# Performance work log

Hardware: AMD Instinct MI355X
Metric: run time of the kernel (lower is better)

## Reference

```python
import jax, jax.numpy as jnp
import numpy as np


def setup_inputs() -> dict:
    key = jax.random.key(0)
    kq, kk, kv = jax.random.split(key, 3)
    B, H, T, D = 2, 8, 8192, 64
    return {
        "Q": jax.random.normal(kq, (B, H, T, D), dtype=jnp.float32),
        "K": jax.random.normal(kk, (B, H, T, D), dtype=jnp.float32),
        "V": jax.random.normal(kv, (B, H, T, D), dtype=jnp.float32),
        "window_size": 512,
    }


def _gather_bands(x, nb, Wn):
    # x: [B,H,T,D] -> [B,H,nb,3*Wn,D], key blocks (i-1, i, i+1) per query block i
    B, H, T, D = x.shape
    xb = x.reshape(B, H, nb, Wn, D)
    xp = jnp.pad(xb, ((0, 0), (0, 0), (1, 1), (0, 0), (0, 0)))
    return jnp.concatenate([xp[:, :, i:i + nb] for i in range(3)], axis=3)


def reference(Q, K, V, window_size):
    # Sliding-window attention: softmax over keys with |q_idx - kv_idx| <= window_size,
    # computed block-sparsely (only the 3 neighboring key blocks per query block).
    B, H, T, D = Q.shape
    Wn = int(window_size)
    assert T % Wn == 0
    nb = T // Wn
    scale = 1.0 / (D ** 0.5)

    Qb = Q.reshape(B, H, nb, Wn, D)
    Kw = _gather_bands(K, nb, Wn)  # [B,H,nb,3W,D]
    Vw = _gather_bands(V, nb, Wn)

    # scores within the band: [B,H,nb,W,3W]
    s = jnp.einsum('bhnqd,bhnkd->bhnqk', Qb, Kw) * scale

    # exact band mask: global q = n*W + q_loc, global kv = (n-1)*W + k_loc
    q_loc = jnp.arange(Wn)[:, None]
    k_loc = jnp.arange(3 * Wn)[None, :]
    band = jnp.abs(q_loc + Wn - k_loc) <= Wn          # [W, 3W]
    kv_g = (jnp.arange(nb)[:, None] - 1) * Wn + jnp.arange(3 * Wn)[None, :]  # [nb, 3W]
    valid = (kv_g >= 0) & (kv_g < T)
    mask = band[None, :, :] & valid[:, None, :]        # [nb, W, 3W]

    s = jnp.where(mask[None, None], s, -jnp.inf)
    p = jax.nn.softmax(s, axis=-1)
    o = jnp.einsum('bhnqk,bhnkd->bhnqd', p, Vw)
    return o.reshape(B, H, T, D)
```

## Files before the change

### kernel.cpp

```cpp
#include <hip/hip_runtime.h>
#include <hip/hip_bf16.h>
#include <stdint.h>

typedef __attribute__((ext_vector_type(8))) short bf16x8;
typedef __attribute__((ext_vector_type(4))) short bf16x4;
typedef __attribute__((ext_vector_type(4))) float f32x4;

#define T_SEQ   8192
#define D_HEAD  64
#define NHEADS  16
#define WIN     512
#define BQ      128
#define BK      64
#define NTILES  (T_SEQ / BK)
#define TILE_E  (BK * D_HEAD)
#define LDSR    72
#define MASKVAL (-1.0e6f)

#define WS_NEEDED ((size_t)2 * NHEADS * T_SEQ * D_HEAD * 2)

#define MFMA16(a,b,c) __builtin_amdgcn_mfma_f32_16x16x16bf16_1k(a,b,c,0,0,0)

extern "C" __device__ __attribute__((const)) float __ocml_native_exp2_f32(float);
__device__ __forceinline__ float fexp2(float x) { return __ocml_native_exp2_f32(x); }

#define GLDS16(g, l) __builtin_amdgcn_global_load_lds( \
    (const __attribute__((address_space(1))) void*)(g), \
    (__attribute__((address_space(3))) void*)(l), 16, 0, 0)

__device__ __forceinline__ short f2bf(float f) {
    union { float f; uint32_t u; } v; v.f = f;
    return (short)((v.u + 0x7FFFu + ((v.u >> 16) & 1u)) >> 16);
}

__device__ __forceinline__ uint32_t pkbf2(float lo, float hi) {
    union { __hip_bfloat162 h; uint32_t u; } c;
    c.h = __float22bfloat162_rn(make_float2(lo, hi));
    return c.u;
}

__global__ __launch_bounds__(256, 2)
void prep_kv(const float* __restrict__ Kg, const float* __restrict__ Vg,
             short* __restrict__ Kb, short* __restrict__ Vt)
{
    __shared__ float vt[64 * 65];
    const int tid  = threadIdx.x;
    const int tile = blockIdx.x & (NTILES - 1);
    const int head = blockIdx.x >> 7;
    const size_t off = ((size_t)head * T_SEQ + (size_t)tile * BK) * D_HEAD;

    const float* ks = Kg + off;
    short* kd = Kb + off;
    #pragma unroll
    for (int i = 0; i < 2; ++i) {
        int L = tid + 256 * i;
        int row = L >> 3, c = L & 7;
        const float* s = ks + row * 64 + c * 8;
        float4 a = *(const float4*)s;
        float4 b = *(const float4*)(s + 4);
        short out[8] = { f2bf(a.x), f2bf(a.y), f2bf(a.z), f2bf(a.w),
                         f2bf(b.x), f2bf(b.y), f2bf(b.z), f2bf(b.w) };
        *(bf16x8*)(kd + (row * 8 + (c ^ (row & 7))) * 8) = *(bf16x8*)out;
    }

    const float* vs = Vg + off;
    #pragma unroll
    for (int i = 0; i < 4; ++i) {
        int idx = tid + 256 * i;
        int row = idx >> 4, c4 = (idx & 15) << 2;
        float4 v = *(const float4*)(vs + row * D_HEAD + c4);
        *(float4*)&vt[row * 65 + c4] = v;
    }
    __syncthreads();
    short* vd = Vt + ((size_t)head * NTILES + tile) * TILE_E;
    {
        int d = tid >> 2, q = tid & 3;
        #pragma unroll
        for (int h = 0; h < 2; ++h) {
            int c = h * 4 + q;
            short out[8];
            #pragma unroll
            for (int j = 0; j < 4; ++j) out[j]     = f2bf(vt[(h*32      + q*4 + j) * 65 + d]);
            #pragma unroll
            for (int j = 0; j < 4; ++j) out[4 + j] = f2bf(vt[(h*32 + 16 + q*4 + j) * 65 + d]);
            *(bf16x8*)(vd + (d * 8 + (c ^ (d & 7))) * 8) = *(bf16x8*)out;
        }
    }
}

__global__ __launch_bounds__(256, 4)
void swa_fwd(const float* __restrict__ Qg, const short* __restrict__ Kb,
             const short* __restrict__ Vt, float* __restrict__ Og)
{
    __shared__ short Ks[2][TILE_E];
    __shared__ short Vs[2][TILE_E];

    const int tid  = threadIdx.x;
    const int wave = tid >> 6;
    const int lane = tid & 63;
    const int lcol = lane & 15;
    const int quad = lane >> 4;
    const int rx   = lcol & 7;

    const int g    = blockIdx.x;
    const int head = g >> 6;
    const int qt   = ((g & 7) << 3) | ((g >> 3) & 7);
    const int q0   = qt * BQ;
    const int tq   = q0 >> 6;

    const float* Qp = Qg + (size_t)head * T_SEQ * D_HEAD;
    const short* Kp = Kb + (size_t)head * T_SEQ * D_HEAD;
    float*       Op = Og + (size_t)head * T_SEQ * D_HEAD;

    const float qscale = 0.125f * 1.44269504088896340736f;
    const int qrow_w = q0 + wave * 32;

    bf16x8 qf[2][2];
    #pragma unroll
    for (int mt = 0; mt < 2; ++mt) {
        const float* qptr = Qp + (size_t)(qrow_w + mt*16 + lcol) * D_HEAD + quad * 8;
        #pragma unroll
        for (int ks = 0; ks < 2; ++ks) {
            float4 a = *(const float4*)(qptr + ks*32);
            float4 b = *(const float4*)(qptr + ks*32 + 4);
            bf16x8 f;
            f[0]=f2bf(a.x*qscale); f[1]=f2bf(a.y*qscale); f[2]=f2bf(a.z*qscale); f[3]=f2bf(a.w*qscale);
            f[4]=f2bf(b.x*qscale); f[5]=f2bf(b.y*qscale); f[6]=f2bf(b.z*qscale); f[7]=f2bf(b.w*qscale);
            qf[mt][ks] = f;
        }
    }

    f32x4 oacc[2][4];
    f32x4 lacc[2];
    const f32x4 zero4 = {0.f, 0.f, 0.f, 0.f};
    const short oneb = (short)0x3F80;
    const bf16x4 ones4 = {oneb, oneb, oneb, oneb};
    #pragma unroll
    for (int mt = 0; mt < 2; ++mt) {
        lacc[mt] = zero4;
        #pragma unroll
        for (int nt = 0; nt < 4; ++nt) oacc[mt][nt] = zero4;
    }

    int t0 = (q0 - WIN) >> 6;            if (t0 < 0) t0 = 0;
    int t1 = (q0 + BQ - 1 + WIN) >> 6;   if (t1 > NTILES - 1) t1 = NTILES - 1;

    const int ch0 = wave * 2, ch1 = wave * 2 + 1;

    {
        const short* ksrc = Kp + (size_t)t0 * TILE_E;
        const short* vsrc = Vt + ((size_t)head * NTILES + t0) * TILE_E;
        GLDS16(ksrc + ch0*512 + lane*8, &Ks[0][ch0*512]);
        GLDS16(ksrc + ch1*512 + lane*8, &Ks[0][ch1*512]);
        GLDS16(vsrc + ch0*512 + lane*8, &Vs[0][ch0*512]);
        GLDS16(vsrc + ch1*512 + lane*8, &Vs[0][ch1*512]);
    }
    asm volatile("s_waitcnt vmcnt(0)" ::: "memory");
    __syncthreads();

    int p = 0;
    for (int t = t0; t <= t1; ++t) {
        {
            const int tn = (t + 1 <= t1) ? t + 1 : t1;
            const short* ksrc = Kp + (size_t)tn * TILE_E;
            const short* vsrc = Vt + ((size_t)head * NTILES + tn) * TILE_E;
            short* kds = &Ks[p^1][0];
            short* vds = &Vs[p^1][0];
            GLDS16(ksrc + ch0*512 + lane*8, kds + ch0*512);
            GLDS16(ksrc + ch1*512 + lane*8, kds + ch1*512);
            GLDS16(vsrc + ch0*512 + lane*8, vds + ch0*512);
            GLDS16(vsrc + ch1*512 + lane*8, vds + ch1*512);
        }

        const short* Kcur = &Ks[p][0];
        const short* Vcur = &Vs[p][0];
        const bool edge = (t < tq - 6) || (t > tq + 7);

        #pragma unroll
        for (int h = 0; h < 2; ++h) {
            bf16x8 vv[4];
            #pragma unroll
            for (int nt = 0; nt < 4; ++nt)
                vv[nt] = *(const bf16x8*)&Vcur[(nt*16 + lcol)*64 + (((h*4 + quad) ^ rx) << 3)];

            f32x4 sc[2][2];
            #pragma unroll
            for (int j = 0; j < 2; ++j) { sc[j][0] = zero4; sc[j][1] = zero4; }
            #pragma unroll
            for (int ks = 0; ks < 2; ++ks) {
                #pragma unroll
                for (int j = 0; j < 2; ++j) {
                    bf16x8 kf = *(const bf16x8*)&Kcur[((2*h+j)*16 + lcol)*64
                                                      + (((ks*4 + quad) ^ rx) << 3)];
                    sc[j][0] = __builtin_amdgcn_mfma_f32_16x16x32_bf16(kf, qf[0][ks], sc[j][0], 0,0,0);
                    sc[j][1] = __builtin_amdgcn_mfma_f32_16x16x32_bf16(kf, qf[1][ks], sc[j][1], 0,0,0);
                }
            }

            if (edge) {
                #pragma unroll
                for (int j = 0; j < 2; ++j) {
                    const int kg0 = t*BK + (2*h+j)*16 + quad*4;
                    #pragma unroll
                    for (int mt = 0; mt < 2; ++mt) {
                        const int qg = qrow_w + mt*16 + lcol;
                        #pragma unroll
                        for (int r = 0; r < 4; ++r) {
                            int dq = qg - (kg0 + r);
                            if (dq > WIN || dq < -WIN) sc[j][mt][r] = MASKVAL;
                        }
                    }
                }
            }

            #pragma unroll
            for (int j = 0; j < 2; ++j) {
                bf16x4 vh[4];
                #pragma unroll
                for (int nt = 0; nt < 4; ++nt) {
                    bf16x8 v8 = vv[nt];
                    bf16x4 x = { v8[j*4+0], v8[j*4+1], v8[j*4+2], v8[j*4+3] };
                    vh[nt] = x;
                }
                #pragma unroll
                for (int mt = 0; mt < 2; ++mt) {
                    float p0 = fexp2(sc[j][mt][0]);
                    float p1 = fexp2(sc[j][mt][1]);
                    float p2 = fexp2(sc[j][mt][2]);
                    float p3 = fexp2(sc[j][mt][3]);
                    union { int2 i; bf16x4 v; } pf;
                    pf.i = make_int2((int)pkbf2(p0, p1), (int)pkbf2(p2, p3));
                    lacc[mt] = MFMA16(ones4, pf.v, lacc[mt]);
                    #pragma unroll
                    for (int nt = 0; nt < 4; ++nt)
                        oacc[mt][nt] = MFMA16(vh[nt], pf.v, oacc[mt][nt]);
                }
            }
        }

        asm volatile("s_waitcnt vmcnt(0)" ::: "memory");
        __syncthreads();
        p ^= 1;
    }

    #pragma unroll
    for (int mt = 0; mt < 2; ++mt) {
        float inv = 1.0f / lacc[mt][0];
        const int qg = qrow_w + mt*16 + lcol;
        float* op = Op + (size_t)qg * D_HEAD + quad*4;
        #pragma unroll
        for (int nt = 0; nt < 4; ++nt) {
            float4 o = { oacc[mt][nt][0]*inv, oacc[mt][nt][1]*inv,
                         oacc[mt][nt][2]*inv, oacc[mt][nt][3]*inv };
            *(float4*)(op + nt*16) = o;
        }
    }
}

#define BQF     128
__global__ __launch_bounds__(256, 4)
void swa_fused_fb(const float* __restrict__ Qg, const float* __restrict__ Kg,
                  const float* __restrict__ Vg, float* __restrict__ Og)
{
    __shared__ short Ksf[BK * LDSR];
    __shared__ short Vsf[D_HEAD * LDSR];
    __shared__ float Vtmp[BK * 65];

    const int tid  = threadIdx.x;
    const int wave = tid >> 6;
    const int lane = tid & 63;
    const int lcol = lane & 15;
    const int quad = lane >> 4;

    const int g    = blockIdx.x;
    const int head = g >> 6;
    const int qt   = ((g & 7) << 3) | ((g >> 3) & 7);
    const int q0   = qt * BQF;
    const int tq   = q0 >> 6;

    const size_t hoff = (size_t)head * T_SEQ * D_HEAD;
    const float* Qp = Qg + hoff;
    const float* Kp = Kg + hoff;
    const float* Vp = Vg + hoff;
    float*       Op = Og + hoff;

    const float qscale = 0.125f * 1.44269504088896340736f;
    const int qrow_w = q0 + wave * 32;

    bf16x8 qf[2][2];
    #pragma unroll
    for (int mt = 0; mt < 2; ++mt) {
        const float* qptr = Qp + (size_t)(qrow_w + mt*16 + lcol) * D_HEAD + quad * 8;
        #pragma unroll
        for (int ks = 0; ks < 2; ++ks) {
            float4 a = *(const float4*)(qptr + ks*32);
            float4 b = *(const float4*)(qptr + ks*32 + 4);
            bf16x8 f;
            f[0]=f2bf(a.x*qscale); f[1]=f2bf(a.y*qscale); f[2]=f2bf(a.z*qscale); f[3]=f2bf(a.w*qscale);
            f[4]=f2bf(b.x*qscale); f[5]=f2bf(b.y*qscale); f[6]=f2bf(b.z*qscale); f[7]=f2bf(b.w*qscale);
            qf[mt][ks] = f;
        }
    }

    f32x4 oacc[2][4];
    float l_run[2];
    const f32x4 zero4 = {0.f, 0.f, 0.f, 0.f};
    #pragma unroll
    for (int mt = 0; mt < 2; ++mt) {
        l_run[mt] = 0.f;
        #pragma unroll
        for (int nt = 0; nt < 4; ++nt) oacc[mt][nt] = zero4;
    }

    int t0 = (q0 - WIN) >> 6;            if (t0 < 0) t0 = 0;
    int t1 = (q0 + BQF - 1 + WIN) >> 6;  if (t1 > NTILES - 1) t1 = NTILES - 1;

    const int krow0 = tid >> 3, kc = (tid & 7) << 3;
    const int krow1 = krow0 + 32;
    const int vrow  = tid >> 4, vc = (tid & 15) << 2;
    const int td    = tid >> 2, tkq = (tid & 3) << 4;

    for (int t = t0; t <= t1; ++t) {
        const float* ksrc = Kp + (size_t)t * BK * D_HEAD;
        const float* vsrc = Vp + (size_t)t * BK * D_HEAD;
        float4 k00 = *(const float4*)(ksrc + krow0*D_HEAD + kc);
        float4 k01 = *(const float4*)(ksrc + krow0*D_HEAD + kc + 4);
        float4 k10 = *(const float4*)(ksrc + krow1*D_HEAD + kc);
        float4 k11 = *(const float4*)(ksrc + krow1*D_HEAD + kc + 4);
        float4 v0  = *(const float4*)(vsrc + (vrow     )*D_HEAD + vc);
        float4 v1  = *(const float4*)(vsrc + (vrow + 16)*D_HEAD + vc);
        float4 v2  = *(const float4*)(vsrc + (vrow + 32)*D_HEAD + vc);
        float4 v3  = *(const float4*)(vsrc + (vrow + 48)*D_HEAD + vc);

        __syncthreads();

        *(float4*)&Vtmp[(vrow     )*65 + vc] = v0;
        *(float4*)&Vtmp[(vrow + 16)*65 + vc] = v1;
        *(float4*)&Vtmp[(vrow + 32)*65 + vc] = v2;
        *(float4*)&Vtmp[(vrow + 48)*65 + vc] = v3;
        *(int4*)&Ksf[krow0*LDSR + kc] = make_int4((int)pkbf2(k00.x,k00.y), (int)pkbf2(k00.z,k00.w),
                                                  (int)pkbf2(k01.x,k01.y), (int)pkbf2(k01.z,k01.w));
        *(int4*)&Ksf[krow1*LDSR + kc] = make_int4((int)pkbf2(k10.x,k10.y), (int)pkbf2(k10.z,k10.w),
                                                  (int)pkbf2(k11.x,k11.y), (int)pkbf2(k11.z,k11.w));

        __syncthreads();

        {
            uint32_t w0 = pkbf2(Vtmp[(tkq+ 0)*65 + td], Vtmp[(tkq+ 1)*65 + td]);
            uint32_t w1 = pkbf2(Vtmp[(tkq+ 2)*65 + td], Vtmp[(tkq+ 3)*65 + td]);
            uint32_t w2 = pkbf2(Vtmp[(tkq+ 4)*65 + td], Vtmp[(tkq+ 5)*65 + td]);
            uint32_t w3 = pkbf2(Vtmp[(tkq+ 6)*65 + td], Vtmp[(tkq+ 7)*65 + td]);
            uint32_t w4 = pkbf2(Vtmp[(tkq+ 8)*65 + td], Vtmp[(tkq+ 9)*65 + td]);
            uint32_t w5 = pkbf2(Vtmp[(tkq+10)*65 + td], Vtmp[(tkq+11)*65 + td]);
            uint32_t w6 = pkbf2(Vtmp[(tkq+12)*65 + td], Vtmp[(tkq+13)*65 + td]);
            uint32_t w7 = pkbf2(Vtmp[(tkq+14)*65 + td], Vtmp[(tkq+15)*65 + td]);
            *(int4*)&Vsf[td*LDSR + tkq]     = make_int4((int)w0,(int)w1,(int)w2,(int)w3);
            *(int4*)&Vsf[td*LDSR + tkq + 8] = make_int4((int)w4,(int)w5,(int)w6,(int)w7);
        }

        __syncthreads();

        const bool edge = (t < tq - 6) || (t > tq + 7);

        #pragma unroll
        for (int h = 0; h < 2; ++h) {
            f32x4 sc[2][2];
            #pragma unroll
            for (int j = 0; j < 2; ++j) { sc[j][0] = zero4; sc[j][1] = zero4; }
            #pragma unroll
            for (int ks = 0; ks < 2; ++ks) {
                #pragma unroll
                for (int j = 0; j < 2; ++j) {
                    bf16x8 kf = *(const bf16x8*)&Ksf[((2*h+j)*16 + lcol)*LDSR + ks*32 + quad*8];
                    sc[j][0] = __builtin_amdgcn_mfma_f32_16x16x32_bf16(kf, qf[0][ks], sc[j][0], 0,0,0);
                    sc[j][1] = __builtin_amdgcn_mfma_f32_16x16x32_bf16(kf, qf[1][ks], sc[j][1], 0,0,0);
                }
            }

            if (edge) {
                #pragma unroll
                for (int j = 0; j < 2; ++j) {
                    const int kg0 = t*BK + (2*h+j)*16 + quad*4;
                    #pragma unroll
                    for (int mt = 0; mt < 2; ++mt) {
                        const int qg = qrow_w + mt*16 + lcol;
                        #pragma unroll
                        for (int r = 0; r < 4; ++r) {
                            int dq = qg - (kg0 + r);
                            if (dq > WIN || dq < -WIN) sc[j][mt][r] = MASKVAL;
                        }
                    }
                }
            }

            #pragma unroll
            for (int j = 0; j < 2; ++j) {
                const int kt = 2*h + j;
                bf16x4 vf[4];
                #pragma unroll
                for (int nt = 0; nt < 4; ++nt)
                    vf[nt] = *(const bf16x4*)&Vsf[(nt*16 + lcol)*LDSR + kt*16 + quad*4];
                #pragma unroll
                for (int mt = 0; mt < 2; ++mt) {
                    float p0 = fexp2(sc[j][mt][0]);
                    float p1 = fexp2(sc[j][mt][1]);
                    float p2 = fexp2(sc[j][mt][2]);
                    float p3 = fexp2(sc[j][mt][3]);
                    l_run[mt] += (p0 + p1) + (p2 + p3);
                    union { int2 i; bf16x4 v; } pf;
                    pf.i = make_int2((int)pkbf2(p0, p1), (int)pkbf2(p2, p3));
                    #pragma unroll
                    for (int nt = 0; nt < 4; ++nt)
                        oacc[mt][nt] = MFMA16(vf[nt], pf.v, oacc[mt][nt]);
                }
            }
        }
    }

    #pragma unroll
    for (int mt = 0; mt < 2; ++mt) {
        float l = l_run[mt];
        l += __shfl_xor(l, 16, 64);
        l += __shfl_xor(l, 32, 64);
        float inv = 1.0f / l;
        const int qg = qrow_w + mt*16 + lcol;
        float* op = Op + (size_t)qg * D_HEAD + quad*4;
        #pragma unroll
        for (int nt = 0; nt < 4; ++nt) {
            float4 o = { oacc[mt][nt][0]*inv, oacc[mt][nt][1]*inv,
                         oacc[mt][nt][2]*inv, oacc[mt][nt][3]*inv };
            *(float4*)(op + nt*16) = o;
        }
    }
}

extern "C" void kernel_launch(void* const* d_in, const int* in_sizes, int n_in,
                              void* d_out, int out_size, void* d_ws, size_t ws_size,
                              hipStream_t stream)
{
    const float* Q = (const float*)d_in[0];
    const float* K = (const float*)d_in[1];
    const float* V = (const float*)d_in[2];
    float* O = (float*)d_out;

    if (ws_size >= WS_NEEDED) {
        short* Kb = (short*)d_ws;
        short* Vt = Kb + (size_t)NHEADS * T_SEQ * D_HEAD;
        prep_kv<<<dim3(NHEADS * NTILES), dim3(256), 0, stream>>>(K, V, Kb, Vt);
        swa_fwd<<<dim3(NHEADS * (T_SEQ / BQ)), dim3(256), 0, stream>>>(Q, Kb, Vt, O);
    } else {
        swa_fused_fb<<<dim3(NHEADS * (T_SEQ / BQF)), dim3(256), 0, stream>>>(Q, K, V, O);
    }
}
```

Before: 183.8 us.

## Split 128-row query tile across 8 waves of 16 rows each

The main attention kernel now launches 512 threads per block, so each of 8 waves owns 16 query rows instead of 4 waves owning 32 rows. Each wave loads one chunk of K and V per tile instead of two. This halves per-wave accumulator registers and the MFMA chain length, aiming for more latency hiding through higher wave occupancy. In exchange, each wave reloads the K/V fragments from LDS for half as many rows, which doubles LDS read traffic per output row, and the 512-thread barrier is larger.

```diff
diff --git a/kernel.cpp b/kernel.cpp
--- a/kernel.cpp
+++ b/kernel.cpp
@@ -88,7 +88,7 @@
     }
 }
 
-__global__ __launch_bounds__(256, 4)
+__global__ __launch_bounds__(512, 8)
 void swa_fwd(const float* __restrict__ Qg, const short* __restrict__ Kb,
              const short* __restrict__ Vt, float* __restrict__ Og)
 {
@@ -111,6 +111,159 @@
     const float* Qp = Qg + (size_t)head * T_SEQ * D_HEAD;
     const short* Kp = Kb + (size_t)head * T_SEQ * D_HEAD;
     float*       Op = Og + (size_t)head * T_SEQ * D_HEAD;
+
+    const float qscale = 0.125f * 1.44269504088896340736f;
+    const int qrow_w = q0 + wave * 16;
+
+    bf16x8 qf[2];
+    {
+        const float* qptr = Qp + (size_t)(qrow_w + lcol) * D_HEAD + quad * 8;
+        #pragma unroll
+        for (int ks = 0; ks < 2; ++ks) {
+            float4 a = *(const float4*)(qptr + ks*32);
+            float4 b = *(const float4*)(qptr + ks*32 + 4);
+            bf16x8 f;
+            f[0]=f2bf(a.x*qscale); f[1]=f2bf(a.y*qscale); f[2]=f2bf(a.z*qscale); f[3]=f2bf(a.w*qscale);
+            f[4]=f2bf(b.x*qscale); f[5]=f2bf(b.y*qscale); f[6]=f2bf(b.z*qscale); f[7]=f2bf(b.w*qscale);
+            qf[ks] = f;
+        }
+    }
+
+    f32x4 oacc[4];
+    f32x4 lacc;
+    const f32x4 zero4 = {0.f, 0.f, 0.f, 0.f};
+    const short oneb = (short)0x3F80;
+    const bf16x4 ones4 = {oneb, oneb, oneb, oneb};
+    lacc = zero4;
+    #pragma unroll
+    for (int nt = 0; nt < 4; ++nt) oacc[nt] = zero4;
+
+    int t0 = (q0 - WIN) >> 6;            if (t0 < 0) t0 = 0;
+    int t1 = (q0 + BQ - 1 + WIN) >> 6;   if (t1 > NTILES - 1) t1 = NTILES - 1;
+
+    const int ch = wave;
+
+    {
+        const short* ksrc = Kp + (size_t)t0 * TILE_E;
+        const short* vsrc = Vt + ((size_t)head * NTILES + t0) * TILE_E;
+        GLDS16(ksrc + ch*512 + lane*8, &Ks[0][ch*512]);
+        GLDS16(vsrc + ch*512 + lane*8, &Vs[0][ch*512]);
+    }
+    asm volatile("s_waitcnt vmcnt(0)" ::: "memory");
+    __syncthreads();
+
+    int p = 0;
+    for (int t = t0; t <= t1; ++t) {
+        {
+            const int tn = (t + 1 <= t1) ? t + 1 : t1;
+            const short* ksrc = Kp + (size_t)tn * TILE_E;
+            const short* vsrc = Vt + ((size_t)head * NTILES + tn) * TILE_E;
+            GLDS16(ksrc + ch*512 + lane*8, &Ks[p^1][ch*512]);
+            GLDS16(vsrc + ch*512 + lane*8, &Vs[p^1][ch*512]);
+        }
+
+        const short* Kcur = &Ks[p][0];
+        const short* Vcur = &Vs[p][0];
+        const bool edge = (t < tq - 6) || (t > tq + 7);
+
+        #pragma unroll
+        for (int h = 0; h < 2; ++h) {
+            bf16x8 vv[4];
+            #pragma unroll
+            for (int nt = 0; nt < 4; ++nt)
+                vv[nt] = *(const bf16x8*)&Vcur[(nt*16 + lcol)*64 + (((h*4 + quad) ^ rx) << 3)];
+
+            f32x4 sc[2];
+            sc[0] = zero4; sc[1] = zero4;
+            #pragma unroll
+            for (int ks = 0; ks < 2; ++ks) {
+                #pragma unroll
+                for (int j = 0; j < 2; ++j) {
+                    bf16x8 kf = *(const bf16x8*)&Kcur[((2*h+j)*16 + lcol)*64
+                                                      + (((ks*4 + quad) ^ rx) << 3)];
+                    sc[j] = __builtin_amdgcn_mfma_f32_16x16x32_bf16(kf, qf[ks], sc[j], 0,0,0);
+                }
+            }
+
+            if (edge) {
+                #pragma unroll
+                for (int j = 0; j < 2; ++j) {
+                    const int kg0 = t*BK + (2*h+j)*16 + quad*4;
+                    const int qg  = qrow_w + lcol;
+                    #pragma unroll
+                    for (int r = 0; r < 4; ++r) {
+                        int dq = qg - (kg0 + r);
+                        if (dq > WIN || dq < -WIN) sc[j][r] = MASKVAL;
+                    }
+                }
+            }
+
+            #pragma unroll
+            for (int j = 0; j < 2; ++j) {
+                bf16x4 vh[4];
+                #pragma unroll
+                for (int nt = 0; nt < 4; ++nt) {
+                    bf16x8 v8 = vv[nt];
+                    bf16x4 x = { v8[j*4+0], v8[j*4+1], v8[j*4+2], v8[j*4+3] };
+                    vh[nt] = x;
+                }
+                float p0 = fexp2(sc[j][0]);
+                float p1 = fexp2(sc[j][1]);
+                float p2 = fexp2(sc[j][2]);
+                float p3 = fexp2(sc[j][3]);
+                union { int2 i; bf16x4 v; } pf;
+                pf.i = make_int2((int)pkbf2(p0, p1), (int)pkbf2(p2, p3));
+                lacc = MFMA16(ones4, pf.v, lacc);
+                #pragma unroll
+                for (int nt = 0; nt < 4; ++nt)
+                    oacc[nt] = MFMA16(vh[nt], pf.v, oacc[nt]);
+            }
+        }
+
+        asm volatile("s_waitcnt vmcnt(0)" ::: "memory");
+        __syncthreads();
+        p ^= 1;
+    }
+
+    {
+        float inv = 1.0f / lacc[0];
+        const int qg = qrow_w + lcol;
+        float* op = Op + (size_t)qg * D_HEAD + quad*4;
+        #pragma unroll
+        for (int nt = 0; nt < 4; ++nt) {
+            float4 o = { oacc[nt][0]*inv, oacc[nt][1]*inv,
+                         oacc[nt][2]*inv, oacc[nt][3]*inv };
+            *(float4*)(op + nt*16) = o;
+        }
+    }
+}
+
+#define BQF     128
+__global__ __launch_bounds__(256, 4)
+void swa_fused_fb(const float* __restrict__ Qg, const float* __restrict__ Kg,
+                  const float* __restrict__ Vg, float* __restrict__ Og)
+{
+    __shared__ short Ksf[BK * LDSR];
+    __shared__ short Vsf[D_HEAD * LDSR];
+    __shared__ float Vtmp[BK * 65];
+
+    const int tid  = threadIdx.x;
+    const int wave = tid >> 6;
+    const int lane = tid & 63;
+    const int lcol = lane & 15;
+    const int quad = lane >> 4;
+
+    const int g    = blockIdx.x;
+    const int head = g >> 6;
+    const int qt   = ((g & 7) << 3) | ((g >> 3) & 7);
+    const int q0   = qt * BQF;
+    const int tq   = q0 >> 6;
+
+    const size_t hoff = (size_t)head * T_SEQ * D_HEAD;
+    const float* Qp = Qg + hoff;
+    const float* Kp = Kg + hoff;
+    const float* Vp = Vg + hoff;
+    float*       Op = Og + hoff;
 
     const float qscale = 0.125f * 1.44269504088896340736f;
     const int qrow_w = q0 + wave * 32;
@@ -131,58 +284,67 @@
     }
 
     f32x4 oacc[2][4];
-    f32x4 lacc[2];
+    float l_run[2];
     const f32x4 zero4 = {0.f, 0.f, 0.f, 0.f};
-    const short oneb = (short)0x3F80;
-    const bf16x4 ones4 = {oneb, oneb, oneb, oneb};
     #pragma unroll
     for (int mt = 0; mt < 2; ++mt) {
-        lacc[mt] = zero4;
+        l_run[mt] = 0.f;
         #pragma unroll
         for (int nt = 0; nt < 4; ++nt) oacc[mt][nt] = zero4;
     }
 
     int t0 = (q0 - WIN) >> 6;            if (t0 < 0) t0 = 0;
-    int t1 = (q0 + BQ - 1 + WIN) >> 6;   if (t1 > NTILES - 1) t1 = NTILES - 1;
-
-    const int ch0 = wave * 2, ch1 = wave * 2 + 1;
-
-    {
-        const short* ksrc = Kp + (size_t)t0 * TILE_E;
-        const short* vsrc = Vt + ((size_t)head * NTILES + t0) * TILE_E;
-        GLDS16(ksrc + ch0*512 + lane*8, &Ks[0][ch0*512]);
-        GLDS16(ksrc + ch1*512 + lane*8, &Ks[0][ch1*512]);
-        GLDS16(vsrc + ch0*512 + lane*8, &Vs[0][ch0*512]);
-        GLDS16(vsrc + ch1*512 + lane*8, &Vs[0][ch1*512]);
-    }
-    asm volatile("s_waitcnt vmcnt(0)" ::: "memory");
-    __syncthreads();
-
-    int p = 0;
+    int t1 = (q0 + BQF - 1 + WIN) >> 6;  if (t1 > NTILES - 1) t1 = NTILES - 1;
+
+    const int krow0 = tid >> 3, kc = (tid & 7) << 3;
+    const int krow1 = krow0 + 32;
+    const int vrow  = tid >> 4, vc = (tid & 15) << 2;
+    const int td    = tid >> 2, tkq = (tid & 3) << 4;
+
     for (int t = t0; t <= t1; ++t) {
+        const float* ksrc = Kp + (size_t)t * BK * D_HEAD;
+        const float* vsrc = Vp + (size_t)t * BK * D_HEAD;
+        float4 k00 = *(const float4*)(ksrc + krow0*D_HEAD + kc);
+        float4 k01 = *(const float4*)(ksrc + krow0*D_HEAD + kc + 4);
+        float4 k10 = *(const float4*)(ksrc + krow1*D_HEAD + kc);
+        float4 k11 = *(const float4*)(ksrc + krow1*D_HEAD + kc + 4);
+        float4 v0  = *(const float4*)(vsrc + (vrow     )*D_HEAD + vc);
+        float4 v1  = *(const float4*)(vsrc + (vrow + 16)*D_HEAD + vc);
+        float4 v2  = *(const float4*)(vsrc + (vrow + 32)*D_HEAD + vc);
+        float4 v3  = *(const float4*)(vsrc + (vrow + 48)*D_HEAD + vc);
+
+        __syncthreads();
+
+        *(float4*)&Vtmp[(vrow     )*65 + vc] = v0;
+        *(float4*)&Vtmp[(vrow + 16)*65 + vc] = v1;
+        *(float4*)&Vtmp[(vrow + 32)*65 + vc] = v2;
+        *(float4*)&Vtmp[(vrow + 48)*65 + vc] = v3;
+        *(int4*)&Ksf[krow0*LDSR + kc] = make_int4((int)pkbf2(k00.x,k00.y), (int)pkbf2(k00.z,k00.w),
+                                                  (int)pkbf2(k01.x,k01.y), (int)pkbf2(k01.z,k01.w));
+        *(int4*)&Ksf[krow1*LDSR + kc] = make_int4((int)pkbf2(k10.x,k10.y), (int)pkbf2(k10.z,k10.w),
+                                                  (int)pkbf2(k11.x,k11.y), (int)pkbf2(k11.z,k11.w));
+
+        __syncthreads();
+
         {
-            const int tn = (t + 1 <= t1) ? t + 1 : t1;
-            const short* ksrc = Kp + (size_t)tn * TILE_E;
-            const short* vsrc = Vt + ((size_t)head * NTILES + tn) * TILE_E;
-            short* kds = &Ks[p^1][0];
-            short* vds = &Vs[p^1][0];
-            GLDS16(ksrc + ch0*512 + lane*8, kds + ch0*512);
-            GLDS16(ksrc + ch1*512 + lane*8, kds + ch1*512);
-            GLDS16(vsrc + ch0*512 + lane*8, vds + ch0*512);
-            GLDS16(vsrc + ch1*512 + lane*8, vds + ch1*512);
-        }
-
-        const short* Kcur = &Ks[p][0];
-        const short* Vcur = &Vs[p][0];
+            uint32_t w0 = pkbf2(Vtmp[(tkq+ 0)*65 + td], Vtmp[(tkq+ 1)*65 + td]);
+            uint32_t w1 = pkbf2(Vtmp[(tkq+ 2)*65 + td], Vtmp[(tkq+ 3)*65 + td]);
+            uint32_t w2 = pkbf2(Vtmp[(tkq+ 4)*65 + td], Vtmp[(tkq+ 5)*65 + td]);
+            uint32_t w3 = pkbf2(Vtmp[(tkq+ 6)*65 + td], Vtmp[(tkq+ 7)*65 + td]);
+            uint32_t w4 = pkbf2(Vtmp[(tkq+ 8)*65 + td], Vtmp[(tkq+ 9)*65 + td]);
+            uint32_t w5 = pkbf2(Vtmp[(tkq+10)*65 + td], Vtmp[(tkq+11)*65 + td]);
+            uint32_t w6 = pkbf2(Vtmp[(tkq+12)*65 + td], Vtmp[(tkq+13)*65 + td]);
+            uint32_t w7 = pkbf2(Vtmp[(tkq+14)*65 + td], Vtmp[(tkq+15)*65 + td]);
+            *(int4*)&Vsf[td*LDSR + tkq]     = make_int4((int)w0,(int)w1,(int)w2,(int)w3);
+            *(int4*)&Vsf[td*LDSR + tkq + 8] = make_int4((int)w4,(int)w5,(int)w6,(int)w7);
+        }
+
+        __syncthreads();
+
         const bool edge = (t < tq - 6) || (t > tq + 7);
 
         #pragma unroll
         for (int h = 0; h < 2; ++h) {
-            bf16x8 vv[4];
-            #pragma unroll
-            for (int nt = 0; nt < 4; ++nt)
-                vv[nt] = *(const bf16x8*)&Vcur[(nt*16 + lcol)*64 + (((h*4 + quad) ^ rx) << 3)];
-
             f32x4 sc[2][2];
             #pragma unroll
             for (int j = 0; j < 2; ++j) { sc[j][0] = zero4; sc[j][1] = zero4; }
@@ -190,8 +352,7 @@
             for (int ks = 0; ks < 2; ++ks) {
                 #pragma unroll
                 for (int j = 0; j < 2; ++j) {
-                    bf16x8 kf = *(const bf16x8*)&Kcur[((2*h+j)*16 + lcol)*64
-                                                      + (((ks*4 + quad) ^ rx) << 3)];
+                    bf16x8 kf = *(const bf16x8*)&Ksf[((2*h+j)*16 + lcol)*LDSR + ks*32 + quad*8];
                     sc[j][0] = __builtin_amdgcn_mfma_f32_16x16x32_bf16(kf, qf[0][ks], sc[j][0], 0,0,0);
                     sc[j][1] = __builtin_amdgcn_mfma_f32_16x16x32_bf16(kf, qf[1][ks], sc[j][1], 0,0,0);
                 }
@@ -215,186 +376,6 @@
 
             #pragma unroll
             for (int j = 0; j < 2; ++j) {
-                bf16x4 vh[4];
-                #pragma unroll
-                for (int nt = 0; nt < 4; ++nt) {
-                    bf16x8 v8 = vv[nt];
-                    bf16x4 x = { v8[j*4+0], v8[j*4+1], v8[j*4+2], v8[j*4+3] };
-                    vh[nt] = x;
-                }
-                #pragma unroll
-                for (int mt = 0; mt < 2; ++mt) {
-                    float p0 = fexp2(sc[j][mt][0]);
-                    float p1 = fexp2(sc[j][mt][1]);
-                    float p2 = fexp2(sc[j][mt][2]);
-                    float p3 = fexp2(sc[j][mt][3]);
-                    union { int2 i; bf16x4 v; } pf;
-                    pf.i = make_int2((int)pkbf2(p0, p1), (int)pkbf2(p2, p3));
-                    lacc[mt] = MFMA16(ones4, pf.v, lacc[mt]);
-                    #pragma unroll
-                    for (int nt = 0; nt < 4; ++nt)
-                        oacc[mt][nt] = MFMA16(vh[nt], pf.v, oacc[mt][nt]);
-                }
-            }
-        }
-
-        asm volatile("s_waitcnt vmcnt(0)" ::: "memory");
-        __syncthreads();
-        p ^= 1;
-    }
-
-    #pragma unroll
-    for (int mt = 0; mt < 2; ++mt) {
-        float inv = 1.0f / lacc[mt][0];
-        const int qg = qrow_w + mt*16 + lcol;
-        float* op = Op + (size_t)qg * D_HEAD + quad*4;
-        #pragma unroll
-        for (int nt = 0; nt < 4; ++nt) {
-            float4 o = { oacc[mt][nt][0]*inv, oacc[mt][nt][1]*inv,
-                         oacc[mt][nt][2]*inv, oacc[mt][nt][3]*inv };
-            *(float4*)(op + nt*16) = o;
-        }
-    }
-}
-
-#define BQF     128
-__global__ __launch_bounds__(256, 4)
-void swa_fused_fb(const float* __restrict__ Qg, const float* __restrict__ Kg,
-                  const float* __restrict__ Vg, float* __restrict__ Og)
-{
-    __shared__ short Ksf[BK * LDSR];
-    __shared__ short Vsf[D_HEAD * LDSR];
-    __shared__ float Vtmp[BK * 65];
-
-    const int tid  = threadIdx.x;
-    const int wave = tid >> 6;
-    const int lane = tid & 63;
-    const int lcol = lane & 15;
-    const int quad = lane >> 4;
-
-    const int g    = blockIdx.x;
-    const int head = g >> 6;
-    const int qt   = ((g & 7) << 3) | ((g >> 3) & 7);
-    const int q0   = qt * BQF;
-    const int tq   = q0 >> 6;
-
-    const size_t hoff = (size_t)head * T_SEQ * D_HEAD;
-    const float* Qp = Qg + hoff;
-    const float* Kp = Kg + hoff;
-    const float* Vp = Vg + hoff;
-    float*       Op = Og + hoff;
-
-    const float qscale = 0.125f * 1.44269504088896340736f;
-    const int qrow_w = q0 + wave * 32;
-
-    bf16x8 qf[2][2];
-    #pragma unroll
-    for (int mt = 0; mt < 2; ++mt) {
-        const float* qptr = Qp + (size_t)(qrow_w + mt*16 + lcol) * D_HEAD + quad * 8;
-        #pragma unroll
-        for (int ks = 0; ks < 2; ++ks) {
-            float4 a = *(const float4*)(qptr + ks*32);
-            float4 b = *(const float4*)(qptr + ks*32 + 4);
-            bf16x8 f;
-            f[0]=f2bf(a.x*qscale); f[1]=f2bf(a.y*qscale); f[2]=f2bf(a.z*qscale); f[3]=f2bf(a.w*qscale);
-            f[4]=f2bf(b.x*qscale); f[5]=f2bf(b.y*qscale); f[6]=f2bf(b.z*qscale); f[7]=f2bf(b.w*qscale);
-            qf[mt][ks] = f;
-        }
-    }
-
-    f32x4 oacc[2][4];
-    float l_run[2];
-    const f32x4 zero4 = {0.f, 0.f, 0.f, 0.f};
-    #pragma unroll
-    for (int mt = 0; mt < 2; ++mt) {
-        l_run[mt] = 0.f;
-        #pragma unroll
-        for (int nt = 0; nt < 4; ++nt) oacc[mt][nt] = zero4;
-    }
-
-    int t0 = (q0 - WIN) >> 6;            if (t0 < 0) t0 = 0;
-    int t1 = (q0 + BQF - 1 + WIN) >> 6;  if (t1 > NTILES - 1) t1 = NTILES - 1;
-
-    const int krow0 = tid >> 3, kc = (tid & 7) << 3;
-    const int krow1 = krow0 + 32;
-    const int vrow  = tid >> 4, vc = (tid & 15) << 2;
-    const int td    = tid >> 2, tkq = (tid & 3) << 4;
-
-    for (int t = t0; t <= t1; ++t) {
-        const float* ksrc = Kp + (size_t)t * BK * D_HEAD;
-        const float* vsrc = Vp + (size_t)t * BK * D_HEAD;
-        float4 k00 = *(const float4*)(ksrc + krow0*D_HEAD + kc);
-        float4 k01 = *(const float4*)(ksrc + krow0*D_HEAD + kc + 4);
-        float4 k10 = *(const float4*)(ksrc + krow1*D_HEAD + kc);
-        float4 k11 = *(const float4*)(ksrc + krow1*D_HEAD + kc + 4);
-        float4 v0  = *(const float4*)(vsrc + (vrow     )*D_HEAD + vc);
-        float4 v1  = *(const float4*)(vsrc + (vrow + 16)*D_HEAD + vc);
-        float4 v2  = *(const float4*)(vsrc + (vrow + 32)*D_HEAD + vc);
-        float4 v3  = *(const float4*)(vsrc + (vrow + 48)*D_HEAD + vc);
-
-        __syncthreads();
-
-        *(float4*)&Vtmp[(vrow     )*65 + vc] = v0;
-        *(float4*)&Vtmp[(vrow + 16)*65 + vc] = v1;
-        *(float4*)&Vtmp[(vrow + 32)*65 + vc] = v2;
-        *(float4*)&Vtmp[(vrow + 48)*65 + vc] = v3;
-        *(int4*)&Ksf[krow0*LDSR + kc] = make_int4((int)pkbf2(k00.x,k00.y), (int)pkbf2(k00.z,k00.w),
-                                                  (int)pkbf2(k01.x,k01.y), (int)pkbf2(k01.z,k01.w));
-        *(int4*)&Ksf[krow1*LDSR + kc] = make_int4((int)pkbf2(k10.x,k10.y), (int)pkbf2(k10.z,k10.w),
-                                                  (int)pkbf2(k11.x,k11.y), (int)pkbf2(k11.z,k11.w));
-
-        __syncthreads();
-
-        {
-            uint32_t w0 = pkbf2(Vtmp[(tkq+ 0)*65 + td], Vtmp[(tkq+ 1)*65 + td]);
-            uint32_t w1 = pkbf2(Vtmp[(tkq+ 2)*65 + td], Vtmp[(tkq+ 3)*65 + td]);
-            uint32_t w2 = pkbf2(Vtmp[(tkq+ 4)*65 + td], Vtmp[(tkq+ 5)*65 + td]);
-            uint32_t w3 = pkbf2(Vtmp[(tkq+ 6)*65 + td], Vtmp[(tkq+ 7)*65 + td]);
-            uint32_t w4 = pkbf2(Vtmp[(tkq+ 8)*65 + td], Vtmp[(tkq+ 9)*65 + td]);
-            uint32_t w5 = pkbf2(Vtmp[(tkq+10)*65 + td], Vtmp[(tkq+11)*65 + td]);
-            uint32_t w6 = pkbf2(Vtmp[(tkq+12)*65 + td], Vtmp[(tkq+13)*65 + td]);
-            uint32_t w7 = pkbf2(Vtmp[(tkq+14)*65 + td], Vtmp[(tkq+15)*65 + td]);
-            *(int4*)&Vsf[td*LDSR + tkq]     = make_int4((int)w0,(int)w1,(int)w2,(int)w3);
-            *(int4*)&Vsf[td*LDSR + tkq + 8] = make_int4((int)w4,(int)w5,(int)w6,(int)w7);
-        }
-
-        __syncthreads();
-
-        const bool edge = (t < tq - 6) || (t > tq + 7);
-
-        #pragma unroll
-        for (int h = 0; h < 2; ++h) {
-            f32x4 sc[2][2];
-            #pragma unroll
-            for (int j = 0; j < 2; ++j) { sc[j][0] = zero4; sc[j][1] = zero4; }
-            #pragma unroll
-            for (int ks = 0; ks < 2; ++ks) {
-                #pragma unroll
-                for (int j = 0; j < 2; ++j) {
-                    bf16x8 kf = *(const bf16x8*)&Ksf[((2*h+j)*16 + lcol)*LDSR + ks*32 + quad*8];
-                    sc[j][0] = __builtin_amdgcn_mfma_f32_16x16x32_bf16(kf, qf[0][ks], sc[j][0], 0,0,0);
-                    sc[j][1] = __builtin_amdgcn_mfma_f32_16x16x32_bf16(kf, qf[1][ks], sc[j][1], 0,0,0);
-                }
-            }
-
-            if (edge) {
-                #pragma unroll
-                for (int j = 0; j < 2; ++j) {
-                    const int kg0 = t*BK + (2*h+j)*16 + quad*4;
-                    #pragma unroll
-                    for (int mt = 0; mt < 2; ++mt) {
-                        const int qg = qrow_w + mt*16 + lcol;
-                        #pragma unroll
-                        for (int r = 0; r < 4; ++r) {
-                            int dq = qg - (kg0 + r);
-                            if (dq > WIN || dq < -WIN) sc[j][mt][r] = MASKVAL;
-                        }
-                    }
-                }
-            }
-
-            #pragma unroll
-            for (int j = 0; j < 2; ++j) {
                 const int kt = 2*h + j;
                 bf16x4 vf[4];
                 #pragma unroll
@@ -447,7 +428,7 @@
         short* Kb = (short*)d_ws;
         short* Vt = Kb + (size_t)NHEADS * T_SEQ * D_HEAD;
         prep_kv<<<dim3(NHEADS * NTILES), dim3(256), 0, stream>>>(K, V, Kb, Vt);
-        swa_fwd<<<dim3(NHEADS * (T_SEQ / BQ)), dim3(256), 0, stream>>>(Q, Kb, Vt, O);
+        swa_fwd<<<dim3(NHEADS * (T_SEQ / BQ)), dim3(512), 0, stream>>>(Q, Kb, Vt, O);
     } else {
         swa_fused_fb<<<dim3(NHEADS * (T_SEQ / BQF)), dim3(256), 0, stream>>>(Q, K, V, O);
     }
```

New measurement: 205.9 us. 1.12x slower.
